# Kernel tuning notes

Measured on AMD Instinct MI355X. Metric: run time of the kernel, lower is better.

## Reference

```python
import jax, jax.numpy as jnp
from jax import lax
import numpy as np

B, A, C = 8, 49104, 90
IMG = 512.0            # 512 + compound_coef*128, coef=0
SCORE_THR = 0.2
IOU_THR = 0.2
K_PRE = 1000           # top candidates kept before NMS (standard TF-style padded NMS)
K_OUT = 100            # max detections per image


def setup_inputs() -> dict:
    key = jax.random.key(0)
    k1, k2, k3, k4, k5, k6 = jax.random.split(key, 6)
    cls_preds = jax.random.uniform(k1, (B, A, C), dtype=jnp.float32)
    loc_preds = 0.1 * jax.random.normal(k2, (B, A, 4), dtype=jnp.float32)
    # plausible anchors in (y1, x1, y2, x2) within the 512x512 image
    cy = jax.random.uniform(k3, (A,)) * IMG
    cx = jax.random.uniform(k4, (A,)) * IMG
    h = 16.0 + jax.random.uniform(k5, (A,)) * 112.0
    w = 16.0 + jax.random.uniform(k6, (A,)) * 112.0
    anchors = jnp.stack([cy - h / 2, cx - w / 2, cy + h / 2, cx + w / 2], axis=-1).astype(jnp.float32)
    return {"cls_preds": cls_preds, "loc_preds": loc_preds, "anchors": anchors}


def _decode_and_clip(anchors, loc_preds):
    # anchors: [A,4] (y1,x1,y2,x2); loc_preds: [B,A,4] (dy,dx,dh,dw)
    ya = (anchors[:, 0] + anchors[:, 2]) / 2
    xa = (anchors[:, 1] + anchors[:, 3]) / 2
    ha = anchors[:, 2] - anchors[:, 0]
    wa = anchors[:, 3] - anchors[:, 1]
    dy, dx, dh, dw = loc_preds[..., 0], loc_preds[..., 1], loc_preds[..., 2], loc_preds[..., 3]
    h = jnp.exp(dh) * ha
    w = jnp.exp(dw) * wa
    yc = dy * ha + ya
    xc = dx * wa + xa
    # output boxes in (xmin, ymin, xmax, ymax), clipped to image
    boxes = jnp.stack([xc - w / 2, yc - h / 2, xc + w / 2, yc + h / 2], axis=-1)
    return jnp.clip(boxes, 0.0, IMG)


def _pairwise_iou(boxes):
    # boxes: [K,4] xyxy -> [K,K]
    x1 = jnp.maximum(boxes[:, None, 0], boxes[None, :, 0])
    y1 = jnp.maximum(boxes[:, None, 1], boxes[None, :, 1])
    x2 = jnp.minimum(boxes[:, None, 2], boxes[None, :, 2])
    y2 = jnp.minimum(boxes[:, None, 3], boxes[None, :, 3])
    inter = jnp.clip(x2 - x1, 0.0) * jnp.clip(y2 - y1, 0.0)
    area = (boxes[:, 2] - boxes[:, 0]) * (boxes[:, 3] - boxes[:, 1])
    return inter / (area[:, None] + area[None, :] - inter + 1e-8)


def _nms_single(scores, classes, boxes):
    # scores: [A], classes: [A] int32, boxes: [A,4]
    masked = jnp.where(scores > SCORE_THR, scores, -1.0)
    vals, idx = lax.top_k(masked, K_PRE)          # top candidates
    b = boxes[idx]                                 # [K_PRE,4]
    cls = classes[idx]                             # [K_PRE]
    # batched_nms trick: offset boxes per class so cross-class IoU is 0
    off = b + cls[:, None].astype(b.dtype) * (IMG + 1.0)
    ious = _pairwise_iou(off)                      # [K_PRE,K_PRE]

    def body(keep, i):
        sup = jnp.any(keep & (ious[:, i] > IOU_THR))
        k = (vals[i] > SCORE_THR) & (~sup)
        return keep.at[i].set(k), None

    keep, _ = lax.scan(body, jnp.zeros((K_PRE,), bool), jnp.arange(K_PRE))
    final = jnp.where(keep, vals, -1.0)
    fvals, fidx = lax.top_k(final, K_OUT)
    det = fvals > 0.0
    out_boxes = jnp.where(det[:, None], b[fidx], jnp.array([0.0, 0.0, 1.0, 1.0], dtype=b.dtype))
    out_scores = jnp.where(det, fvals, 0.0)
    out_labels = jnp.where(det, cls[fidx], -1)
    return out_boxes, out_scores, out_labels


def reference(cls_preds, loc_preds, anchors):
    boxes = _decode_and_clip(anchors, loc_preds)   # [B,A,4]
    scores = jnp.max(cls_preds, axis=2)            # [B,A]
    classes = jnp.argmax(cls_preds, axis=2).astype(jnp.int32)
    out_boxes, out_scores, out_labels = jax.vmap(_nms_single)(scores, classes, boxes)
    return out_boxes, out_scores, out_labels
```

## Files before the change

### kernel.cpp

```cpp
#include <hip/hip_runtime.h>
#include <stdint.h>

#define B_    8
#define A_    49104
#define C_    90
#define IMG_  512.0f
#define THR_  0.2f
#define KPRE  1000
#define KOUT  100
#define NCAND 1024
#define NKEY  2048
#define NBIN  1024
#define BINBASE 0x17C99u
#define THRU    0xBE4CCCCDu
#define GANCH 64

static __device__ __forceinline__ uint32_t f2ord(float f) {
    uint32_t b = __float_as_uint(f);
    return (b & 0x80000000u) ? ~b : (b | 0x80000000u);
}
static __device__ __forceinline__ float ord2f(uint32_t u) {
    uint32_t b = (u & 0x80000000u) ? (u & 0x7FFFFFFFu) : ~u;
    return __uint_as_float(b);
}

__global__ __launch_bounds__(256)
void k_score_decode(const float* __restrict__ cls,
                    const float* __restrict__ loc,
                    const float* __restrict__ anc,
                    uint32_t* __restrict__ scores_u,
                    int* __restrict__ classes,
                    float* __restrict__ boxes) {
    __shared__ float4 s4[(GANCH * C_) / 4];
    __shared__ float r_val[GANCH];
    __shared__ int   r_cls[GANCH];

    int tid = threadIdx.x;
    int b = blockIdx.y;
    int a0 = blockIdx.x * GANCH;
    int valid = A_ - a0; if (valid > GANCH) valid = GANCH;

    const float4* src = (const float4*)(cls + (size_t)(b * A_ + a0) * C_);
    if (valid == GANCH) {
        float4 v0 = src[tid];
        float4 v1 = src[tid + 256];
        float4 v2 = src[tid + 512];
        float4 v3 = src[tid + 768];
        float4 v4 = src[tid + 1024];
        float4 v5;
        if (tid < 160) v5 = src[tid + 1280];
        s4[tid]        = v0;
        s4[tid + 256]  = v1;
        s4[tid + 512]  = v2;
        s4[tid + 768]  = v3;
        s4[tid + 1024] = v4;
        if (tid < 160) s4[tid + 1280] = v5;
    } else {
        int n4 = (valid * C_) / 4;
        for (int i = tid; i < n4; i += 256) s4[i] = src[i];
    }
    __syncthreads();

    const float* s = (const float*)s4;
    int g = tid >> 2, sub = tid & 3;
    float best = -1.0f; int bi = 0;
    if (g < valid) {
        #pragma unroll
        for (int j = sub; j < C_ + 2; j += 4) {
            if (j < C_) {
                float v = s[g * C_ + j];
                if (v > best) { best = v; bi = j; }
            }
        }
    }
    #pragma unroll
    for (int d = 1; d < 4; d <<= 1) {
        float ov = __shfl_xor(best, d);
        int   oi = __shfl_xor(bi, d);
        if (ov > best || (ov == best && oi < bi)) { best = ov; bi = oi; }
    }
    if (sub == 0 && g < valid) { r_val[g] = best; r_cls[g] = bi; }
    __syncthreads();

    if (tid < valid) {
        int a = a0 + tid;
        int gid = b * A_ + a;
        float bv = r_val[tid];
        float m = (bv > THR_) ? bv : -1.0f;
        scores_u[gid] = f2ord(m);
        classes[gid]  = r_cls[tid];

        float4 an = ((const float4*)anc)[a];
        float4 l4 = ((const float4*)loc)[gid];
        float ya = (an.x + an.z) * 0.5f;
        float xa = (an.y + an.w) * 0.5f;
        float ha = an.z - an.x;
        float wa = an.w - an.y;
        float h  = expf(l4.z) * ha;
        float w  = expf(l4.w) * wa;
        float yc = l4.x * ha + ya;
        float xc = l4.y * wa + xa;
        float4 bx;
        bx.x = fminf(fmaxf(xc - w * 0.5f, 0.0f), IMG_);
        bx.y = fminf(fmaxf(yc - h * 0.5f, 0.0f), IMG_);
        bx.z = fminf(fmaxf(xc + w * 0.5f, 0.0f), IMG_);
        bx.w = fminf(fmaxf(yc + h * 0.5f, 0.0f), IMG_);
        ((float4*)boxes)[gid] = bx;
    }
}

__global__ __launch_bounds__(1024)
void k_seltop(const uint32_t* __restrict__ scores_u,
              const int* __restrict__ classes,
              const float* __restrict__ boxes,
              float* __restrict__ cand_val,
              int* __restrict__ cand_cls,
              float* __restrict__ cand_box,
              int* __restrict__ n_valid) {
    int b = blockIdx.x;
    int t = threadIdx.x;
    int lane = t & 63;
    __shared__ uint64_t keys[NKEY];
    __shared__ uint32_t h[NBIN];
    __shared__ uint32_t sh_coarse;
    __shared__ int      sh_rem;
    __shared__ uint32_t sh_cutoff;
    __shared__ int      sh_cnt;
    const uint32_t* su = scores_u + (size_t)b * A_;
    const uint32_t PREF = f2ord(0.9997f);

    if (t == 0) sh_cnt = 0;
    __syncthreads();

    const uint4* su4 = (const uint4*)su;
    for (int i = t; i < A_ / 4; i += 1024) {
        uint4 v = su4[i];
        #pragma unroll
        for (int c = 0; c < 4; ++c) {
            uint32_t u = (c == 0) ? v.x : (c == 1) ? v.y : (c == 2) ? v.z : v.w;
            unsigned long long m = __ballot(u >= PREF);
            if (m) {
                uint32_t base;
                if (lane == 0) base = atomicAdd((uint32_t*)&sh_cnt, (uint32_t)__popcll(m));
                base = __shfl((int)base, 0);
                if (u >= PREF) {
                    int p = (int)base +
                            (int)__popcll(m & ((1ull << lane) - 1ull));
                    if (p < NKEY)
                        keys[p] = ((uint64_t)u << 32) |
                                  (uint32_t)(~(uint32_t)(4 * i + c));
                }
            }
        }
    }
    __syncthreads();
    int n = sh_cnt;

    if (n < KPRE || n > NKEY) {
        h[t] = 0;
        if (t == 0) sh_cnt = 0;
        __syncthreads();
        for (int a = t; a < A_; a += 1024) {
            uint32_t u = su[a];
            if (u > THRU) {
                int bin = (int)(u >> 15) - (int)BINBASE;
                bin = bin < 0 ? 0 : (bin >= NBIN ? NBIN - 1 : bin);
                atomicAdd(&h[bin], 1u);
            }
        }
        __syncthreads();
        for (int d = 1; d < NBIN; d <<= 1) {
            uint32_t add = (t + d < NBIN) ? h[t + d] : 0u;
            __syncthreads();
            h[t] += add;
            __syncthreads();
        }
        {
            uint32_t St = h[t];
            uint32_t Sn = (t + 1 < NBIN) ? h[t + 1] : 0u;
            if (St >= KPRE && Sn < KPRE) {
                sh_coarse = (BINBASE + (uint32_t)t) << 15;
                sh_rem = KPRE - (int)Sn;
            }
            if (t == 0 && h[0] < KPRE) {
                sh_rem = 0;
                sh_coarse = 0xFFFFFFFFu;
                sh_cutoff = BINBASE << 15;
            }
        }
        __syncthreads();
        uint32_t coarse = sh_coarse;
        int rem = sh_rem;

        h[t] = 0;
        __syncthreads();
        if (rem > 0) {
            for (int a = t; a < A_; a += 1024) {
                uint32_t u = su[a];
                if ((u & 0xFFFF8000u) == coarse)
                    atomicAdd(&h[(u >> 5) & 0x3FF], 1u);
            }
        }
        __syncthreads();
        for (int d = 1; d < NBIN; d <<= 1) {
            uint32_t add = (t + d < NBIN) ? h[t + d] : 0u;
            __syncthreads();
            h[t] += add;
            __syncthreads();
        }
        if (rem > 0) {
            int St = (int)h[t];
            int Sn = (t + 1 < NBIN) ? (int)h[t + 1] : 0;
            if (St >= rem && Sn < rem)
                sh_cutoff = coarse | ((uint32_t)t << 5);
        }
        __syncthreads();
        uint32_t cutoff = sh_cutoff;

        for (int a = t; a < A_; a += 1024) {
            uint32_t u = su[a];
            if (u >= cutoff) {
                int p = atomicAdd(&sh_cnt, 1);
                if (p < NKEY)
                    keys[p] = ((uint64_t)u << 32) | (uint32_t)(~(uint32_t)a);
            }
        }
        __syncthreads();
        n = sh_cnt; if (n > NKEY) n = NKEY;
    }

    uint64_t k0 = (t        < n) ? keys[t]        : 0ull;
    uint64_t k1 = (t + 1024 < n) ? keys[t + 1024] : 0ull;
    int r0 = 0, r1 = 0;
    #pragma unroll 4
    for (int j = 0; j < n; ++j) {
        uint64_t v = keys[j];
        r0 += (v > k0);
        r1 += (v > k1);
    }
    #pragma unroll
    for (int q = 0; q < 2; ++q) {
        int i = t + q * 1024;
        int r = q == 0 ? r0 : r1;
        uint64_t k = q == 0 ? k0 : k1;
        if (i < n && r < NCAND) {
            uint32_t u = (uint32_t)(k >> 32);
            int ai = (int)(~(uint32_t)k);
            int ci = b * NCAND + r;
            cand_val[ci] = ord2f(u);
            cand_cls[ci] = classes[(size_t)b * A_ + ai];
            ((float4*)cand_box)[ci] = ((const float4*)boxes)[(size_t)b * A_ + ai];
        }
    }
    int nn = n < NCAND ? n : NCAND;
    for (int i = nn + t; i < NCAND; i += 1024) {
        int ci = b * NCAND + i;
        cand_val[ci] = -1.0f;
        cand_cls[ci] = 0;
        float4 z; z.x = z.y = z.z = z.w = 0.0f;
        ((float4*)cand_box)[ci] = z;
    }
    if (t == 0) n_valid[b] = n < KPRE ? n : KPRE;
}

__global__ void k_masks(const float* __restrict__ cand_box,
                        const int* __restrict__ cand_cls,
                        unsigned short* __restrict__ M16) {
    int b = blockIdx.x;
    __shared__ float x1s[NCAND], y1s[NCAND], x2s[NCAND], y2s[NCAND], ars[NCAND];
    for (int i = threadIdx.x; i < NCAND; i += blockDim.x) {
        int ci = b * NCAND + i;
        float4 bx = ((const float4*)cand_box)[ci];
        float off = (float)cand_cls[ci] * (IMG_ + 1.0f);
        float ox1 = bx.x + off, oy1 = bx.y + off;
        float ox2 = bx.z + off, oy2 = bx.w + off;
        x1s[i] = ox1; y1s[i] = oy1; x2s[i] = ox2; y2s[i] = oy2;
        ars[i] = (ox2 - ox1) * (oy2 - oy1);
    }
    __syncthreads();

    int row0 = blockIdx.y * 63;
    for (int item = threadIdx.x; item < 63 * 64; item += blockDim.x) {
        int i = row0 + (item >> 6);
        if (i >= KPRE) continue;
        int w = item & 63;
        if (w < (i >> 4)) continue;
        float xi1 = x1s[i], yi1 = y1s[i], xi2 = x2s[i], yi2 = y2s[i], ai = ars[i];
        unsigned int m = 0;
        int j0 = w * 16;
        #pragma unroll
        for (int t = 0; t < 16; ++t) {
            int j = j0 + t;
            float xx1 = fmaxf(xi1, x1s[j]);
            float yy1 = fmaxf(yi1, y1s[j]);
            float xx2 = fminf(xi2, x2s[j]);
            float yy2 = fminf(yi2, y2s[j]);
            float iw = xx2 - xx1; iw = iw > 0.0f ? iw : 0.0f;
            float ih = yy2 - yy1; ih = ih > 0.0f ? ih : 0.0f;
            float inter = iw * ih;
            float den = (ai + ars[j]) - inter + 1e-8f;
            float iou = inter / den;
            m |= (iou > THR_ ? 1u : 0u) << t;
        }
        M16[((size_t)(b * NCAND + i)) * 64 + w] = (unsigned short)m;
    }
}

__global__ void k_nms_out(const unsigned short* __restrict__ M16,
                          const float* __restrict__ cand_val,
                          const int* __restrict__ cand_cls,
                          const float* __restrict__ cand_box,
                          const int* __restrict__ n_valid,
                          float* __restrict__ out) {
    int b = blockIdx.x;
    int lane = threadIdx.x;
    int nv = n_valid[b]; if (nv > KPRE) nv = KPRE;
    const unsigned short* Mr = M16 + (size_t)b * NCAND * 64;
    __shared__ int kept[KOUT];

    uint32_t S = 0;
    int cnt = 0;
    uint32_t cur[8], nxt[8];
    #pragma unroll
    for (int t = 0; t < 8; ++t) cur[t] = Mr[(size_t)t * 64 + lane];

    for (int base = 0; base < nv && cnt < KOUT; base += 8) {
        #pragma unroll
        for (int t = 0; t < 8; ++t) {
            int r = base + 8 + t;
            nxt[t] = Mr[(size_t)(r < NCAND ? r : 0) * 64 + lane];
        }
        #pragma unroll
        for (int t = 0; t < 8; ++t) {
            int i = base + t;
            bool inb = (i < nv) && (cnt < KOUT);
            unsigned long long ball =
                __ballot(inb && (((S >> (i & 15)) & 1u) != 0u));
            int sup = (int)((ball >> (i >> 4)) & 1ull);
            if (inb && !sup) {
                S |= cur[t];
                if (lane == 0) kept[cnt] = i;
                cnt++;
            }
        }
        #pragma unroll
        for (int t = 0; t < 8; ++t) cur[t] = nxt[t];
    }
    __syncthreads();

    for (int s_ = lane; s_ < KOUT; s_ += 64) {
        float b0 = 0.0f, b1 = 0.0f, b2 = 1.0f, b3 = 1.0f, sc = 0.0f, lb = -1.0f;
        if (s_ < cnt) {
            int i = kept[s_];
            int ci = b * NCAND + i;
            float4 bx = ((const float4*)cand_box)[ci];
            b0 = bx.x; b1 = bx.y; b2 = bx.z; b3 = bx.w;
            sc = cand_val[ci];
            lb = (float)cand_cls[ci];
        }
        int ob = (b * KOUT + s_) * 4;
        out[ob + 0] = b0; out[ob + 1] = b1; out[ob + 2] = b2; out[ob + 3] = b3;
        out[B_ * KOUT * 4 + b * KOUT + s_] = sc;
        out[B_ * KOUT * 5 + b * KOUT + s_] = lb;
    }
}

extern "C" void kernel_launch(void* const* d_in, const int* in_sizes, int n_in,
                              void* d_out, int out_size, void* d_ws, size_t ws_size,
                              hipStream_t stream) {
    const float* cls = (const float*)d_in[0];
    const float* loc = (const float*)d_in[1];
    const float* anc = (const float*)d_in[2];
    float* out = (float*)d_out;

    char* ws = (char*)d_ws;
    size_t off = 0;
    auto alloc = [&](size_t bytes) -> void* {
        void* p = ws + off;
        off += (bytes + 255) & ~(size_t)255;
        return p;
    };
    uint32_t* scores_u = (uint32_t*)alloc((size_t)B_ * A_ * 4);
    int*      classes  = (int*)     alloc((size_t)B_ * A_ * 4);
    float*    boxes    = (float*)   alloc((size_t)B_ * A_ * 4 * 4);
    float*    cand_val = (float*)   alloc((size_t)B_ * NCAND * 4);
    int*      cand_cls = (int*)     alloc((size_t)B_ * NCAND * 4);
    float*    cand_box = (float*)   alloc((size_t)B_ * NCAND * 4 * 4);
    int*      n_valid  = (int*)     alloc((size_t)B_ * 4);
    unsigned short* M16 = (unsigned short*)alloc((size_t)B_ * NCAND * 64 * 2);

    dim3 gD((A_ + GANCH - 1) / GANCH, B_);
    k_score_decode<<<gD, 256, 0, stream>>>(
        cls, loc, anc, scores_u, classes, boxes);
    k_seltop<<<B_, 1024, 0, stream>>>(
        scores_u, classes, boxes, cand_val, cand_cls, cand_box, n_valid);
    k_masks<<<dim3(B_, 16), 256, 0, stream>>>(cand_box, cand_cls, M16);
    k_nms_out<<<B_, 64, 0, stream>>>(
        M16, cand_val, cand_cls, cand_box, n_valid, out);
}
```

Before: 312.2 us.

## Compact top candidates in score kernel, decode boxes only for selected candidates

The score kernel now writes packed keys (score, anchor index, class) for high-scoring anchors straight into a global buffer using a global atomic counter. It no longer writes per-anchor classes or decoded boxes. The selection kernel loads that compacted buffer, sorts it with a shared-memory bitonic sort in place of the O(n^2) rank count, and decodes boxes only for the surviving candidates. The IoU mask kernel pads its shared arrays to avoid bank conflicts. This removes large global writes and reads of per-anchor boxes and classes, at the cost of global atomics, a memset, and a slower fallback path that recomputes argmax per candidate.

```diff
diff --git a/kernel.cpp b/kernel.cpp
--- a/kernel.cpp
+++ b/kernel.cpp
@@ -14,6 +14,10 @@
 #define BINBASE 0x17C99u
 #define THRU    0xBE4CCCCDu
 #define GANCH 64
+#define PREF_F 0.9997f
+
+#define NPAD 1088
+#define PADI(j) ((j) + ((j) >> 4))
 
 static __device__ __forceinline__ uint32_t f2ord(float f) {
     uint32_t b = __float_as_uint(f);
@@ -25,12 +29,10 @@
 }
 
 __global__ __launch_bounds__(256)
-void k_score_decode(const float* __restrict__ cls,
-                    const float* __restrict__ loc,
-                    const float* __restrict__ anc,
-                    uint32_t* __restrict__ scores_u,
-                    int* __restrict__ classes,
-                    float* __restrict__ boxes) {
+void k_score_compact(const float* __restrict__ cls,
+                     uint32_t* __restrict__ scores_u,
+                     uint64_t* __restrict__ keybuf,
+                     uint32_t* __restrict__ cntg) {
     __shared__ float4 s4[(GANCH * C_) / 4];
     __shared__ float r_val[GANCH];
     __shared__ int   r_cls[GANCH];
@@ -82,81 +84,61 @@
     if (sub == 0 && g < valid) { r_val[g] = best; r_cls[g] = bi; }
     __syncthreads();
 
-    if (tid < valid) {
+    if (tid < 64) {
         int a = a0 + tid;
-        int gid = b * A_ + a;
-        float bv = r_val[tid];
-        float m = (bv > THR_) ? bv : -1.0f;
-        scores_u[gid] = f2ord(m);
-        classes[gid]  = r_cls[tid];
-
-        float4 an = ((const float4*)anc)[a];
-        float4 l4 = ((const float4*)loc)[gid];
-        float ya = (an.x + an.z) * 0.5f;
-        float xa = (an.y + an.w) * 0.5f;
-        float ha = an.z - an.x;
-        float wa = an.w - an.y;
-        float h  = expf(l4.z) * ha;
-        float w  = expf(l4.w) * wa;
-        float yc = l4.x * ha + ya;
-        float xc = l4.y * wa + xa;
-        float4 bx;
-        bx.x = fminf(fmaxf(xc - w * 0.5f, 0.0f), IMG_);
-        bx.y = fminf(fmaxf(yc - h * 0.5f, 0.0f), IMG_);
-        bx.z = fminf(fmaxf(xc + w * 0.5f, 0.0f), IMG_);
-        bx.w = fminf(fmaxf(yc + h * 0.5f, 0.0f), IMG_);
-        ((float4*)boxes)[gid] = bx;
+        bool v = tid < valid;
+        float bv = v ? r_val[tid] : -1.0f;
+        if (v) {
+            float m = (bv > THR_) ? bv : -1.0f;
+            scores_u[b * A_ + a] = f2ord(m);
+        }
+        bool flag = v && (bv >= PREF_F);
+        unsigned long long mb = __ballot(flag);
+        if (mb) {
+            uint32_t base = 0;
+            if (tid == 0) base = atomicAdd(&cntg[b], (uint32_t)__popcll(mb));
+            base = (uint32_t)__shfl((int)base, 0);
+            if (flag) {
+                int p = (int)base + (int)__popcll(mb & ((1ull << tid) - 1ull));
+                if (p < NKEY) {
+                    uint64_t key = ((uint64_t)f2ord(bv) << 32)
+                                 | ((uint64_t)((~(uint32_t)a) & 0xFFFFu) << 16)
+                                 | ((uint64_t)(uint32_t)r_cls[tid] << 8);
+                    keybuf[b * NKEY + p] = key;
+                }
+            }
+        }
     }
 }
 
 __global__ __launch_bounds__(1024)
-void k_seltop(const uint32_t* __restrict__ scores_u,
-              const int* __restrict__ classes,
-              const float* __restrict__ boxes,
-              float* __restrict__ cand_val,
-              int* __restrict__ cand_cls,
-              float* __restrict__ cand_box,
-              int* __restrict__ n_valid) {
+void k_seltop2(const uint32_t* __restrict__ scores_u,
+               const float* __restrict__ cls,
+               const float* __restrict__ loc,
+               const float* __restrict__ anc,
+               const uint64_t* __restrict__ keybuf,
+               const uint32_t* __restrict__ cntg,
+               float* __restrict__ cand_val,
+               int* __restrict__ cand_cls,
+               float* __restrict__ cand_box,
+               int* __restrict__ n_valid) {
     int b = blockIdx.x;
     int t = threadIdx.x;
-    int lane = t & 63;
     __shared__ uint64_t keys[NKEY];
-    __shared__ uint32_t h[NBIN];
     __shared__ uint32_t sh_coarse;
     __shared__ int      sh_rem;
     __shared__ uint32_t sh_cutoff;
     __shared__ int      sh_cnt;
     const uint32_t* su = scores_u + (size_t)b * A_;
-    const uint32_t PREF = f2ord(0.9997f);
-
-    if (t == 0) sh_cnt = 0;
-    __syncthreads();
-
-    const uint4* su4 = (const uint4*)su;
-    for (int i = t; i < A_ / 4; i += 1024) {
-        uint4 v = su4[i];
-        #pragma unroll
-        for (int c = 0; c < 4; ++c) {
-            uint32_t u = (c == 0) ? v.x : (c == 1) ? v.y : (c == 2) ? v.z : v.w;
-            unsigned long long m = __ballot(u >= PREF);
-            if (m) {
-                uint32_t base;
-                if (lane == 0) base = atomicAdd((uint32_t*)&sh_cnt, (uint32_t)__popcll(m));
-                base = __shfl((int)base, 0);
-                if (u >= PREF) {
-                    int p = (int)base +
-                            (int)__popcll(m & ((1ull << lane) - 1ull));
-                    if (p < NKEY)
-                        keys[p] = ((uint64_t)u << 32) |
-                                  (uint32_t)(~(uint32_t)(4 * i + c));
-                }
-            }
-        }
-    }
-    __syncthreads();
-    int n = sh_cnt;
-
-    if (n < KPRE || n > NKEY) {
+
+    int n = (int)cntg[b];
+    bool fast = (n >= KPRE && n <= NKEY);
+
+    if (fast) {
+        for (int i = t; i < NKEY; i += 1024)
+            keys[i] = (i < n) ? keybuf[b * NKEY + i] : 0ull;
+    } else {
+        uint32_t* h = (uint32_t*)keys;
         h[t] = 0;
         if (t == 0) sh_cnt = 0;
         __syncthreads();
@@ -216,45 +198,68 @@
         }
         __syncthreads();
         uint32_t cutoff = sh_cutoff;
+        __syncthreads();
 
         for (int a = t; a < A_; a += 1024) {
             uint32_t u = su[a];
             if (u >= cutoff) {
                 int p = atomicAdd(&sh_cnt, 1);
                 if (p < NKEY)
-                    keys[p] = ((uint64_t)u << 32) | (uint32_t)(~(uint32_t)a);
+                    keys[p] = ((uint64_t)u << 32)
+                            | ((uint64_t)((~(uint32_t)a) & 0xFFFFu) << 16);
             }
         }
         __syncthreads();
         n = sh_cnt; if (n > NKEY) n = NKEY;
-    }
-
-    uint64_t k0 = (t        < n) ? keys[t]        : 0ull;
-    uint64_t k1 = (t + 1024 < n) ? keys[t + 1024] : 0ull;
-    int r0 = 0, r1 = 0;
-    #pragma unroll 4
-    for (int j = 0; j < n; ++j) {
-        uint64_t v = keys[j];
-        r0 += (v > k0);
-        r1 += (v > k1);
-    }
-    #pragma unroll
-    for (int q = 0; q < 2; ++q) {
-        int i = t + q * 1024;
-        int r = q == 0 ? r0 : r1;
-        uint64_t k = q == 0 ? k0 : k1;
-        if (i < n && r < NCAND) {
-            uint32_t u = (uint32_t)(k >> 32);
-            int ai = (int)(~(uint32_t)k);
-            int ci = b * NCAND + r;
-            cand_val[ci] = ord2f(u);
-            cand_cls[ci] = classes[(size_t)b * A_ + ai];
-            ((float4*)cand_box)[ci] = ((const float4*)boxes)[(size_t)b * A_ + ai];
-        }
-    }
-    int nn = n < NCAND ? n : NCAND;
-    for (int i = nn + t; i < NCAND; i += 1024) {
-        int ci = b * NCAND + i;
+        for (int i = t; i < NKEY; i += 1024)
+            if (i >= n) keys[i] = 0ull;
+    }
+    __syncthreads();
+
+    for (int kk = 2; kk <= NKEY; kk <<= 1) {
+        for (int jj = kk >> 1; jj > 0; jj >>= 1) {
+            int i1 = ((t & ~(jj - 1)) << 1) | (t & (jj - 1));
+            int i2 = i1 + jj;
+            uint64_t va = keys[i1], vb = keys[i2];
+            bool desc = ((i1 & kk) == 0);
+            if ((va < vb) == desc) { keys[i1] = vb; keys[i2] = va; }
+            __syncthreads();
+        }
+    }
+
+    uint64_t key = keys[t];
+    bool real = (t < n);
+    int ci = b * NCAND + t;
+    if (real) {
+        int a = (int)((~(uint32_t)(key >> 16)) & 0xFFFFu);
+        int c;
+        if (fast) {
+            c = (int)((key >> 8) & 0xFFu);
+        } else {
+            const float* row = cls + ((size_t)b * A_ + a) * C_;
+            float bb = -1.0f; int bc = 0;
+            for (int j = 0; j < C_; ++j) { float q = row[j]; if (q > bb) { bb = q; bc = j; } }
+            c = bc;
+        }
+        float4 an = ((const float4*)anc)[a];
+        float4 l4 = ((const float4*)loc)[(size_t)b * A_ + a];
+        float ya = (an.x + an.z) * 0.5f;
+        float xa = (an.y + an.w) * 0.5f;
+        float ha = an.z - an.x;
+        float wa = an.w - an.y;
+        float hh = expf(l4.z) * ha;
+        float ww = expf(l4.w) * wa;
+        float yc = l4.x * ha + ya;
+        float xc = l4.y * wa + xa;
+        float4 bx;
+        bx.x = fminf(fmaxf(xc - ww * 0.5f, 0.0f), IMG_);
+        bx.y = fminf(fmaxf(yc - hh * 0.5f, 0.0f), IMG_);
+        bx.z = fminf(fmaxf(xc + ww * 0.5f, 0.0f), IMG_);
+        bx.w = fminf(fmaxf(yc + hh * 0.5f, 0.0f), IMG_);
+        cand_val[ci] = ord2f((uint32_t)(key >> 32));
+        cand_cls[ci] = c;
+        ((float4*)cand_box)[ci] = bx;
+    } else {
         cand_val[ci] = -1.0f;
         cand_cls[ci] = 0;
         float4 z; z.x = z.y = z.z = z.w = 0.0f;
@@ -267,15 +272,16 @@
                         const int* __restrict__ cand_cls,
                         unsigned short* __restrict__ M16) {
     int b = blockIdx.x;
-    __shared__ float x1s[NCAND], y1s[NCAND], x2s[NCAND], y2s[NCAND], ars[NCAND];
+    __shared__ float x1s[NPAD], y1s[NPAD], x2s[NPAD], y2s[NPAD], ars[NPAD];
     for (int i = threadIdx.x; i < NCAND; i += blockDim.x) {
         int ci = b * NCAND + i;
         float4 bx = ((const float4*)cand_box)[ci];
         float off = (float)cand_cls[ci] * (IMG_ + 1.0f);
         float ox1 = bx.x + off, oy1 = bx.y + off;
         float ox2 = bx.z + off, oy2 = bx.w + off;
-        x1s[i] = ox1; y1s[i] = oy1; x2s[i] = ox2; y2s[i] = oy2;
-        ars[i] = (ox2 - ox1) * (oy2 - oy1);
+        int ip = PADI(i);
+        x1s[ip] = ox1; y1s[ip] = oy1; x2s[ip] = ox2; y2s[ip] = oy2;
+        ars[ip] = (ox2 - ox1) * (oy2 - oy1);
     }
     __syncthreads();
 
@@ -285,22 +291,23 @@
         if (i >= KPRE) continue;
         int w = item & 63;
         if (w < (i >> 4)) continue;
-        float xi1 = x1s[i], yi1 = y1s[i], xi2 = x2s[i], yi2 = y2s[i], ai = ars[i];
+        int ip = PADI(i);
+        float xi1 = x1s[ip], yi1 = y1s[ip], xi2 = x2s[ip], yi2 = y2s[ip], ai = ars[ip];
         unsigned int m = 0;
         int j0 = w * 16;
         #pragma unroll
-        for (int t = 0; t < 16; ++t) {
-            int j = j0 + t;
-            float xx1 = fmaxf(xi1, x1s[j]);
-            float yy1 = fmaxf(yi1, y1s[j]);
-            float xx2 = fminf(xi2, x2s[j]);
-            float yy2 = fminf(yi2, y2s[j]);
+        for (int q = 0; q < 16; ++q) {
+            int jp = PADI(j0 + q);
+            float xx1 = fmaxf(xi1, x1s[jp]);
+            float yy1 = fmaxf(yi1, y1s[jp]);
+            float xx2 = fminf(xi2, x2s[jp]);
+            float yy2 = fminf(yi2, y2s[jp]);
             float iw = xx2 - xx1; iw = iw > 0.0f ? iw : 0.0f;
             float ih = yy2 - yy1; ih = ih > 0.0f ? ih : 0.0f;
             float inter = iw * ih;
-            float den = (ai + ars[j]) - inter + 1e-8f;
+            float den = (ai + ars[jp]) - inter + 1e-8f;
             float iou = inter / den;
-            m |= (iou > THR_ ? 1u : 0u) << t;
+            m |= (iou > THR_ ? 1u : 0u) << q;
         }
         M16[((size_t)(b * NCAND + i)) * 64 + w] = (unsigned short)m;
     }
@@ -381,19 +388,21 @@
         return p;
     };
     uint32_t* scores_u = (uint32_t*)alloc((size_t)B_ * A_ * 4);
-    int*      classes  = (int*)     alloc((size_t)B_ * A_ * 4);
-    float*    boxes    = (float*)   alloc((size_t)B_ * A_ * 4 * 4);
+    uint64_t* keybuf   = (uint64_t*)alloc((size_t)B_ * NKEY * 8);
+    uint32_t* cntg     = (uint32_t*)alloc((size_t)B_ * 4);
     float*    cand_val = (float*)   alloc((size_t)B_ * NCAND * 4);
     int*      cand_cls = (int*)     alloc((size_t)B_ * NCAND * 4);
     float*    cand_box = (float*)   alloc((size_t)B_ * NCAND * 4 * 4);
     int*      n_valid  = (int*)     alloc((size_t)B_ * 4);
     unsigned short* M16 = (unsigned short*)alloc((size_t)B_ * NCAND * 64 * 2);
 
+    hipMemsetAsync(cntg, 0, (size_t)B_ * 4, stream);
+
     dim3 gD((A_ + GANCH - 1) / GANCH, B_);
-    k_score_decode<<<gD, 256, 0, stream>>>(
-        cls, loc, anc, scores_u, classes, boxes);
-    k_seltop<<<B_, 1024, 0, stream>>>(
-        scores_u, classes, boxes, cand_val, cand_cls, cand_box, n_valid);
+    k_score_compact<<<gD, 256, 0, stream>>>(cls, scores_u, keybuf, cntg);
+    k_seltop2<<<B_, 1024, 0, stream>>>(
+        scores_u, cls, loc, anc, keybuf, cntg,
+        cand_val, cand_cls, cand_box, n_valid);
     k_masks<<<dim3(B_, 16), 256, 0, stream>>>(cand_box, cand_cls, M16);
     k_nms_out<<<B_, 64, 0, stream>>>(
         M16, cand_val, cand_cls, cand_box, n_valid, out);
```

Result: faster. 282.6 us (-9.5%).
